# Optimization experiments

Measured on AMD Instinct MI355X. Metric: run time of the kernel, lower is better.

Reference implementation:

```python
import jax, jax.numpy as jnp
import numpy as np

B, IC, N = 32, 1, 64
KN, KS, PAD = 128, 65, 16
R, LAT = 8, 32
LEAK = 0.01
THETA_PRIOR = float(np.pi)
HW = N + 2 * PAD - KS + 1  # 32
OFFSETS = np.array([0, np.pi/4, np.pi/2, 3*np.pi/4, np.pi, -3*np.pi/4, -np.pi/2, -np.pi/4], dtype=np.float32)


def rotate_filters(w, n_rot):
    """Bilinear rotation of [O,I,k,k] filters for n_rot angles, matching
    F.affine_grid/F.grid_sample with align_corners=False, zero padding.
    Returns [O*n_rot, I, k, k] (rotation-major within each O block)."""
    O, I, k, _ = w.shape
    thetas = (2.0 * jnp.pi / n_rot) * jnp.arange(n_rot, dtype=jnp.float32)
    coords = (2.0 * jnp.arange(k, dtype=jnp.float32) + 1.0) / k - 1.0  # normalized, align_corners=False
    yy, xx = jnp.meshgrid(coords, coords, indexing='ij')  # [k,k]
    cos = jnp.cos(thetas)[:, None, None]
    sin = jnp.sin(thetas)[:, None, None]
    xs = cos * xx + sin * yy   # [R,k,k] sample x (normalized)
    ys = -sin * xx + cos * yy  # [R,k,k] sample y
    px = ((xs + 1.0) * k - 1.0) * 0.5  # pixel coords
    py = ((ys + 1.0) * k - 1.0) * 0.5
    x0 = jnp.floor(px); y0 = jnp.floor(py)
    wx = px - x0; wy = py - y0

    def gather(yi, xi):
        valid = (yi >= 0) & (yi < k) & (xi >= 0) & (xi < k)
        yc = jnp.clip(yi, 0, k - 1).astype(jnp.int32)
        xc = jnp.clip(xi, 0, k - 1).astype(jnp.int32)
        v = w[:, :, yc, xc]  # [O,I,R,k,k]
        return v * valid.astype(w.dtype)

    out = (gather(y0, x0) * (1 - wy) * (1 - wx)
           + gather(y0, x0 + 1) * (1 - wy) * wx
           + gather(y0 + 1, x0) * wy * (1 - wx)
           + gather(y0 + 1, x0 + 1) * wy * wx)  # [O,I,R,k,k]
    return jnp.transpose(out, (0, 2, 1, 3, 4)).reshape(O * n_rot, I, k, k)


def conv1x1(h, w, b):
    # h: [B,C,R,H,W], w: [O,C], b: [O] -- Conv3d with 1x1x1 kernel
    return jnp.einsum('bcrhw,oc->borhw', h, w) + b[None, :, None, None, None]


def _forward(x, w1, b1, w2, b2, wa, ba, wr, br, wz, bz, gumbel):
    tw = rotate_filters(w1[:, :, 0], R)  # [KN*R, IC, KS, KS]
    y = jax.lax.conv_general_dilated(
        x, tw, window_strides=(1, 1), padding=[(PAD, PAD), (PAD, PAD)],
        dimension_numbers=('NCHW', 'OIHW', 'NCHW'))
    Bn = y.shape[0]
    y = y.reshape(Bn, KN, R, HW, HW) + b1[None, :, None, None, None]
    xa = jax.nn.leaky_relu(y, LEAK)
    h = jax.nn.leaky_relu(conv1x1(xa, w2, b2), LEAK)
    attn = conv1x1(h, wa, ba)[:, 0]  # [B,R,H,W]
    offsets = jnp.asarray(OFFSETS)
    # Normal(0, theta_prior).log_prob(offsets)
    p_r = (-0.5 * (offsets / THETA_PRIOR) ** 2
           - jnp.log(THETA_PRIOR) - 0.5 * jnp.log(2.0 * jnp.pi))[:, None, None]  # [R,1,1]
    attn = attn + p_r  # broadcast over batch
    flat = attn.reshape(Bn, -1)
    q_t_r = jax.nn.log_softmax(flat, axis=1).reshape(attn.shape)
    a_sampled = jax.nn.softmax(flat + gumbel.reshape(Bn, -1), axis=-1).reshape(Bn, R, HW, HW)
    z = conv1x1(h, wz, bz)      # [B,2*LAT,R,H,W]
    theta = conv1x1(h, wr, br)  # [B,2,R,H,W]
    theta_mu = theta[:, 0] + offsets[None, :, None, None]
    theta = jnp.stack((theta_mu, theta[:, 1]), axis=1)
    return attn, q_t_r, p_r, a_sampled, offsets, theta, z


def setup_inputs():
    key = jax.random.key(0)
    ks = jax.random.split(key, 12)
    stdv1 = 1.0 / np.sqrt(IC * KS * KS)
    stdv2 = 1.0 / np.sqrt(KN)
    def unif(k, shape, a):
        return jax.random.uniform(k, shape, jnp.float32, -a, a)
    u = jax.random.uniform(ks[11], (B, R, HW, HW), jnp.float32, 1e-6, 1.0 - 1e-6)
    gumbel = -jnp.log(-jnp.log(u))
    return {
        'x': jax.random.normal(ks[0], (B, IC, N, N), jnp.float32),
        'w1': unif(ks[1], (KN, IC, 1, KS, KS), stdv1),
        'b1': unif(ks[2], (KN,), stdv1),
        'w2': unif(ks[3], (KN, KN), stdv2),
        'b2': unif(ks[4], (KN,), stdv2),
        'wa': unif(ks[5], (1, KN), stdv2),
        'ba': unif(ks[6], (1,), stdv2),
        'wr': unif(ks[7], (2, KN), stdv2),
        'br': unif(ks[8], (2,), stdv2),
        'wz': unif(ks[9], (2 * LAT, KN), stdv2),
        'bz': unif(ks[10], (2 * LAT,), stdv2),
        'gumbel': gumbel,
    }


def reference(x, w1, b1, w2, b2, wa, ba, wr, br, wz, bz, gumbel):
    return _forward(x, w1, b1, w2, b2, wa, ba, wr, br, wz, bz, gumbel)
```

## Files before the change

### kernel.cpp

```cpp
#include <hip/hip_runtime.h>
#include <hip/hip_bf16.h>

typedef unsigned int u32;
typedef unsigned short u16;

#define KYP 72
#define KPAD 4736
#define NK   74

#define OUT_ATTN 0
#define OUT_QTR  262144
#define OUT_PR   524288
#define OUT_AS   524296
#define OUT_OFF  786440
#define OUT_TH   786448
#define OUT_Z    1310736

typedef __attribute__((ext_vector_type(8))) short bf16x8;
typedef __attribute__((ext_vector_type(4))) float f32x4;

__device__ const float OFFS[8] = {
  0.0f,
  0.78539816339744830961f,
  1.57079632679489661923f,
  2.35619449019234492885f,
  3.14159265358979323846f,
 -2.35619449019234492885f,
 -1.57079632679489661923f,
 -0.78539816339744830961f
};

__device__ __forceinline__ float leaky_(float v){ return v >= 0.0f ? v : 0.01f*v; }

__device__ __forceinline__ u16 f2bf(float f){
  u32 x = __float_as_uint(f);
  u32 r = (x + 0x7FFFu + ((x >> 16) & 1u)) >> 16;
  return (u16)r;
}

__device__ __forceinline__ void gload_lds16(const void* g, void* l){
  __builtin_amdgcn_global_load_lds((const __attribute__((address_space(1))) u32*)g,
                                   (__attribute__((address_space(3))) u32*)l, 16, 0, 0);
}

#define BARRIER() { asm volatile("" ::: "memory"); __builtin_amdgcn_s_barrier(); asm volatile("" ::: "memory"); }
#define WAITV(N)  asm volatile("s_waitcnt vmcnt(" #N ")" ::: "memory")
#define LGK0()    { asm volatile("s_waitcnt lgkmcnt(0)" ::: "memory"); __builtin_amdgcn_sched_barrier(0); }

__global__ __launch_bounds__(256) void prep_kernel(const float* __restrict__ x, u16* __restrict__ xsh,
                                                   const float* __restrict__ w1, u16* __restrict__ twb){
  __shared__ float wsh[4225];
  if (blockIdx.x < 1024){
    int n = blockIdx.x;
    int kn = n & 127, rot = n >> 7;
    for (int i = threadIdx.x; i < 4225; i += 256) wsh[i] = w1[kn*4225 + i];
    __syncthreads();
    float th  = 0.78539816339744830961f * (float)rot;
    float cth = cosf(th), sth = sinf(th);
    for (int t = threadIdx.x; t < KPAD; t += 256){
      int ky = t / KYP, kx = t - ky*KYP;
      u16 outv = 0;
      if (ky < 65 && kx < 65){
        float yy = (2.0f*(float)ky + 1.0f)/65.0f - 1.0f;
        float xx = (2.0f*(float)kx + 1.0f)/65.0f - 1.0f;
        float xs  =  cth*xx + sth*yy;
        float ysv = -sth*xx + cth*yy;
        float px = ((xs  + 1.0f)*65.0f - 1.0f)*0.5f;
        float py = ((ysv + 1.0f)*65.0f - 1.0f)*0.5f;
        float x0 = floorf(px), y0 = floorf(py);
        float wx = px - x0, wy = py - y0;
        auto samp = [&](float yf, float xf)->float{
          bool valid = (yf >= 0.0f) && (yf < 65.0f) && (xf >= 0.0f) && (xf < 65.0f);
          int yc = (int)fminf(fmaxf(yf, 0.0f), 64.0f);
          int xc = (int)fminf(fmaxf(xf, 0.0f), 64.0f);
          return valid ? wsh[yc*65 + xc] : 0.0f;
        };
        float val = samp(y0,      x0     )*(1.0f-wy)*(1.0f-wx)
                  + samp(y0,      x0+1.0f)*(1.0f-wy)*wx
                  + samp(y0+1.0f, x0     )*wy*(1.0f-wx)
                  + samp(y0+1.0f, x0+1.0f)*wy*wx;
        outv = f2bf(val);
      }
      twb[(size_t)n*KPAD + t] = outv;
    }
  } else {
    int t = (blockIdx.x - 1024)*256 + threadIdx.x;
    if (t >= 393216) return;
    int c8  = t & 15;
    int u   = t >> 4;
    int row = u % 96;
    int v   = u / 96;
    int b   = v & 31;
    int s   = v >> 5;
    int iy = row - 16;
    u16 h[8];
#pragma unroll
    for (int j = 0; j < 8; ++j){
      int ix = c8*8 + j + s - 16;
      float val = 0.0f;
      if (iy >= 0 && iy < 64 && ix >= 0 && ix < 64) val = x[(b*64 + iy)*64 + ix];
      h[j] = f2bf(val);
    }
    uint4 pk;
    pk.x = (u32)h[0] | ((u32)h[1] << 16);
    pk.y = (u32)h[2] | ((u32)h[3] << 16);
    pk.z = (u32)h[4] | ((u32)h[5] << 16);
    pk.w = (u32)h[6] | ((u32)h[7] << 16);
    ((uint4*)xsh)[t] = pk;
  }
}

__global__ __launch_bounds__(512, 2) void gemm_kernel(const u16* __restrict__ xsh,
                                                      const u16* __restrict__ twb,
                                                      u16* __restrict__ ys){
  __shared__ u16 AsB[2*16384];
  __shared__ u16 BsB[2*16384];

  const int bid  = blockIdx.x;
  const int nblk = bid & 3, mblk = bid >> 2;
  const int t    = threadIdx.x;
  const int lane = t & 63, w = t >> 6;
  const int wr   = w >> 2, wn = w & 3;
  const int hi8  = (lane >> 4) << 3;

  const int sr  = t >> 3;
  const int j0e = (t & 7) * 8;
  const int jsw = j0e ^ ((sr & 7) << 3);
  const int bg  = mblk >> 4;
  const int ox2 = (mblk & 15) * 2;
  int aOff[4];
#pragma unroll
  for (int c = 0; c < 4; ++c){
    int i  = c*64 + sr;
    int ox = ox2 + (i >> 7);
    int s_ = ox & 7, colb = ox & ~7;
    int b_ = (bg << 2) + ((i & 127) >> 5);
    int oy = i & 31;
    aOff[c] = ((s_*32 + b_)*96 + oy)*128 + colb;
  }
  const u16* bPtr[4];
#pragma unroll
  for (int c = 0; c < 4; ++c){
    int nloc = c*64 + sr;
    bPtr[c] = twb + (size_t)(nblk*256 + nloc)*KPAD + jsw;
  }

  auto stageA4 = [&](int ky, int kx0, u16* dstbase){
    bool pad = (ky >= 65);
    int kofs = ky*128 + kx0;
#pragma unroll
    for (int c = 0; c < 4; ++c){
      int gofs = pad ? 0 : (aOff[c] + kofs);
      gload_lds16(xsh + gofs, dstbase + c*4096 + w*512);
    }
  };
  auto stageB4 = [&](int kt, u16* dstbase){
    int ktc = (kt < NK) ? kt : (NK-1);
#pragma unroll
    for (int c = 0; c < 4; ++c)
      gload_lds16(bPtr[c] + ktc*64, dstbase + c*4096 + w*512);
  };

  f32x4 acc[8][4];
#pragma unroll
  for (int i = 0; i < 8; ++i)
#pragma unroll
    for (int j = 0; j < 4; ++j) acc[i][j] = (f32x4){0.f,0.f,0.f,0.f};
  bf16x8 amat[4][2], bmat[4][2];

  auto readA = [&](int mh, const char* Ab){
#pragma unroll
    for (int mj = 0; mj < 4; ++mj){
      int row = wr*128 + mh*64 + mj*16 + (lane & 15);
#pragma unroll
      for (int kk = 0; kk < 2; ++kk){
        int off = (row*128 + (kk*32 + hi8)*2) ^ ((row & 7) << 4);
        amat[mj][kk] = *(const bf16x8*)(Ab + off);
      }
    }
  };
  auto readB = [&](int nh, const char* Bb){
#pragma unroll
    for (int jn = 0; jn < 2; ++jn){
      int row = wn*64 + (nh*2 + jn)*16 + (lane & 15);
#pragma unroll
      for (int kk = 0; kk < 2; ++kk){
        int off = (row*128 + (kk*32 + hi8)*2) ^ ((row & 7) << 4);
        bmat[nh*2 + jn][kk] = *(const bf16x8*)(Bb + off);
      }
    }
  };
  auto mfma16 = [&](int MH, int NH){
    __builtin_amdgcn_s_setprio(1);
#pragma unroll
    for (int mj = 0; mj < 4; ++mj)
#pragma unroll
      for (int jn = 0; jn < 2; ++jn)
#pragma unroll
        for (int kk = 0; kk < 2; ++kk)
          acc[MH*4+mj][NH*2+jn] = __builtin_amdgcn_mfma_f32_16x16x32_bf16(
              amat[mj][kk], bmat[NH*2+jn][kk], acc[MH*4+mj][NH*2+jn], 0, 0, 0);
    __builtin_amdgcn_s_setprio(0);
  };

  u16* const A0 = AsB;
  u16* const B0 = BsB;
  u16* const A1 = AsB + 16384;
  u16* const B1 = BsB + 16384;

  stageB4(0, B0);
  stageA4(0, jsw, A0);
  int kyN = (64 + jsw >= KYP) ? 1 : 0;
  int kxN = 64 + jsw - (kyN ? KYP : 0);
  WAITV(0);
  BARRIER();

  for (int kt = 0; kt < NK; ++kt){
    u16* Ab = (kt & 1) ? A1 : A0;
    u16* Bb = (kt & 1) ? B1 : B0;
    u16* An = (kt & 1) ? A0 : A1;
    u16* Bn = (kt & 1) ? B0 : B1;
    readA(0, (const char*)Ab); readB(0, (const char*)Bb);
    stageB4(kt+1, Bn);
    LGK0();
    mfma16(0, 0);
    readB(1, (const char*)Bb);
    stageA4(kyN, kxN, An);
    LGK0();
    mfma16(0, 1);
    readA(1, (const char*)Ab);
    LGK0();
    mfma16(1, 1);
    mfma16(1, 0);
    kxN += 64; if (kxN >= KYP){ kxN -= KYP; ++kyN; }
    WAITV(0);
    BARRIER();
  }

  const int m_base = mblk*256 + wr*128;
  const int n_base = nblk*256 + wn*64;
  const int rsub = (lane >> 4) << 2;
  const int csub = lane & 15;
#pragma unroll
  for (int mf = 0; mf < 8; ++mf)
#pragma unroll
    for (int nf = 0; nf < 4; ++nf)
#pragma unroll
      for (int j = 0; j < 4; ++j){
        int m = m_base + mf*16 + rsub + j;
        int n = n_base + nf*16 + csub;
        ys[(size_t)m*1024 + n] = f2bf(acc[mf][nf][j]);
      }
}

__global__ __launch_bounds__(512) void mix_kernel(const u16* __restrict__ ys,
    const float* __restrict__ b1, const float* __restrict__ w2, const float* __restrict__ b2,
    const float* __restrict__ wa, const float* __restrict__ ba,
    const float* __restrict__ wr, const float* __restrict__ br,
    const float* __restrict__ wz, const float* __restrict__ bz,
    float* __restrict__ out){
  __shared__ __align__(16) u16 Ah[256*128];
  __shared__ __align__(16) u16 W2s[128*128];
  __shared__ __align__(16) u16 Wcs[80*128];
  __shared__ float b2s[128];
  __shared__ float bcs[80];

  const int blk = blockIdx.x;
  const int b   = blk >> 5, oy = blk & 31;
  const int t    = threadIdx.x;
  const int lane = t & 63;
  const int w    = t >> 6;

  {
    const int kn0 = (t & 15)*8;
    const int r_  = (t >> 4) & 7;
    float b1v[8];
#pragma unroll
    for (int j = 0; j < 8; ++j) b1v[j] = b1[kn0 + j];
#pragma unroll
    for (int i = 0; i < 8; ++i){
      int m_loc = 4*i + (t >> 7);
      int row_m = (((b >> 2)*32 + m_loc)*128) + (b & 3)*32 + oy;
      uint4 v = *(const uint4*)(ys + (size_t)row_m*1024 + r_*128 + kn0);
      u32 vv[4] = {v.x, v.y, v.z, v.w};
      u16 hh[8];
#pragma unroll
      for (int j = 0; j < 4; ++j){
        float lo = __uint_as_float(vv[j] << 16);
        float hi = __uint_as_float(vv[j] & 0xFFFF0000u);
        hh[2*j]   = f2bf(leaky_(lo + b1v[2*j]));
        hh[2*j+1] = f2bf(leaky_(hi + b1v[2*j+1]));
      }
      int Arow = r_*32 + m_loc;
      int off = (Arow*256 + kn0*2) ^ ((Arow & 7) << 4);
      uint4 pk;
      pk.x = (u32)hh[0] | ((u32)hh[1] << 16);
      pk.y = (u32)hh[2] | ((u32)hh[3] << 16);
      pk.z = (u32)hh[4] | ((u32)hh[5] << 16);
      pk.w = (u32)hh[6] | ((u32)hh[7] << 16);
      *(uint4*)((char*)Ah + off) = pk;
    }
  }
#pragma unroll
  for (int i = 0; i < 4; ++i){
    int ch = i*512 + t;
    int row = ch >> 4, kn0 = (ch & 15)*8;
    const float* src = w2 + row*128 + kn0;
    u16 hh[8];
#pragma unroll
    for (int j = 0; j < 8; ++j) hh[j] = f2bf(src[j]);
    int off = (row*256 + kn0*2) ^ ((row & 7) << 4);
    uint4 pk;
    pk.x = (u32)hh[0] | ((u32)hh[1] << 16);
    pk.y = (u32)hh[2] | ((u32)hh[3] << 16);
    pk.z = (u32)hh[4] | ((u32)hh[5] << 16);
    pk.w = (u32)hh[6] | ((u32)hh[7] << 16);
    *(uint4*)((char*)W2s + off) = pk;
  }
#pragma unroll
  for (int i = 0; i < 3; ++i){
    int ch = i*512 + t;
    if (ch < 1280){
      int row = ch >> 4, kn0 = (ch & 15)*8;
      const float* src = nullptr;
      if (row < 64)      src = wz + row*128 + kn0;
      else if (row == 64) src = wa + kn0;
      else if (row == 65) src = wr + kn0;
      else if (row == 66) src = wr + 128 + kn0;
      u16 hh[8];
#pragma unroll
      for (int j = 0; j < 8; ++j) hh[j] = src ? f2bf(src[j]) : (u16)0;
      int off = (row*256 + kn0*2) ^ ((row & 7) << 4);
      uint4 pk;
      pk.x = (u32)hh[0] | ((u32)hh[1] << 16);
      pk.y = (u32)hh[2] | ((u32)hh[3] << 16);
      pk.z = (u32)hh[4] | ((u32)hh[5] << 16);
      pk.w = (u32)hh[6] | ((u32)hh[7] << 16);
      *(uint4*)((char*)Wcs + off) = pk;
    }
  }
  if (t < 128) b2s[t] = b2[t];
  if (t < 80){
    float v = 0.0f;
    if (t < 64) v = bz[t];
    else if (t == 64) v = ba[0];
    else if (t == 65) v = br[0];
    else if (t == 66) v = br[1];
    bcs[t] = v;
  }
  __syncthreads();

  f32x4 acc1[2][8];
#pragma unroll
  for (int mf = 0; mf < 2; ++mf)
#pragma unroll
    for (int nf = 0; nf < 8; ++nf) acc1[mf][nf] = (f32x4){0.f,0.f,0.f,0.f};
#pragma unroll
  for (int kk = 0; kk < 128; kk += 32){
    int kb = (kk + ((lane >> 4) << 3))*2;
    bf16x8 a[2], bv[8];
#pragma unroll
    for (int mf = 0; mf < 2; ++mf){
      int row = w*32 + mf*16 + (lane & 15);
      int off = (row*256 + kb) ^ ((row & 7) << 4);
      a[mf] = *(const bf16x8*)((const char*)Ah + off);
    }
#pragma unroll
    for (int nf = 0; nf < 8; ++nf){
      int row = nf*16 + (lane & 15);
      int off = (row*256 + kb) ^ ((row & 7) << 4);
      bv[nf] = *(const bf16x8*)((const char*)W2s + off);
    }
#pragma unroll
    for (int mf = 0; mf < 2; ++mf)
#pragma unroll
      for (int nf = 0; nf < 8; ++nf)
        acc1[mf][nf] = __builtin_amdgcn_mfma_f32_16x16x32_bf16(a[mf], bv[nf], acc1[mf][nf], 0, 0, 0);
  }
  __syncthreads();

#pragma unroll
  for (int mf = 0; mf < 2; ++mf)
#pragma unroll
    for (int nf = 0; nf < 8; ++nf){
      int col = nf*16 + (lane & 15);
      float bb = b2s[col];
#pragma unroll
      for (int j = 0; j < 4; ++j){
        int row = w*32 + mf*16 + ((lane >> 4) << 2) + j;
        u16 hv = f2bf(leaky_(acc1[mf][nf][j] + bb));
        int off = (row*256 + col*2) ^ ((row & 7) << 4);
        *(u16*)((char*)Ah + off) = hv;
      }
    }
  __syncthreads();

  f32x4 acc2[2][5];
#pragma unroll
  for (int mf = 0; mf < 2; ++mf)
#pragma unroll
    for (int nf = 0; nf < 5; ++nf) acc2[mf][nf] = (f32x4){0.f,0.f,0.f,0.f};
#pragma unroll
  for (int kk = 0; kk < 128; kk += 32){
    int kb = (kk + ((lane >> 4) << 3))*2;
    bf16x8 a[2], bv[5];
#pragma unroll
    for (int mf = 0; mf < 2; ++mf){
      int row = w*32 + mf*16 + (lane & 15);
      int off = (row*256 + kb) ^ ((row & 7) << 4);
      a[mf] = *(const bf16x8*)((const char*)Ah + off);
    }
#pragma unroll
    for (int nf = 0; nf < 5; ++nf){
      int row = nf*16 + (lane & 15);
      int off = (row*256 + kb) ^ ((row & 7) << 4);
      bv[nf] = *(const bf16x8*)((const char*)Wcs + off);
    }
#pragma unroll
    for (int mf = 0; mf < 2; ++mf)
#pragma unroll
      for (int nf = 0; nf < 5; ++nf)
        acc2[mf][nf] = __builtin_amdgcn_mfma_f32_16x16x32_bf16(a[mf], bv[nf], acc2[mf][nf], 0, 0, 0);
  }

  const int r = w;
  float off_r = OFFS[r];
  float qn = off_r / 3.14159265358979323846f;
  float pr = -0.5f*qn*qn - 1.14472988584940017414f - 0.91893853320467274178f;
  const int pixb = oy*32;
#pragma unroll
  for (int mf = 0; mf < 2; ++mf)
#pragma unroll
    for (int nf = 0; nf < 5; ++nf){
      int c = nf*16 + (lane & 15);
#pragma unroll
      for (int j = 0; j < 4; ++j){
        int ox = mf*16 + ((lane >> 4) << 2) + j;
        float val = acc2[mf][nf][j];
        if (c < 64){
          out[OUT_Z + (size_t)b*524288 + (size_t)c*8192 + r*1024 + pixb + ox] = val + bcs[c];
        } else if (c == 64){
          out[OUT_ATTN + (size_t)(b*8 + r)*1024 + pixb + ox] = val + bcs[64] + pr;
        } else if (c == 65){
          out[OUT_TH + ((size_t)b*2)*8192 + r*1024 + pixb + ox] = val + bcs[65] + off_r;
        } else if (c == 66){
          out[OUT_TH + ((size_t)b*2 + 1)*8192 + r*1024 + pixb + ox] = val + bcs[66];
        }
      }
    }
}

__global__ __launch_bounds__(1024) void softmax_kernel(const float* __restrict__ gumbel, float* __restrict__ out){
  __shared__ float a[8192];
  __shared__ float red[1024];
  const int b = blockIdx.x, t = threadIdx.x;
  if (b == 0 && t < 8){
    float off = OFFS[t];
    out[OUT_OFF + t] = off;
    float qn = off / 3.14159265358979323846f;
    out[OUT_PR + t] = -0.5f*qn*qn - 1.14472988584940017414f - 0.91893853320467274178f;
  }
  const float* attn = out + OUT_ATTN + (size_t)b*8192;
  float m = -3.0e38f;
  for (int i = t; i < 8192; i += 1024){ float v = attn[i]; a[i] = v; m = fmaxf(m, v); }
  red[t] = m; __syncthreads();
#pragma unroll
  for (int s = 512; s > 0; s >>= 1){ if (t < s) red[t] = fmaxf(red[t], red[t+s]); __syncthreads(); }
  m = red[0]; __syncthreads();
  float s1 = 0.0f;
  for (int i = t; i < 8192; i += 1024) s1 += expf(a[i] - m);
  red[t] = s1; __syncthreads();
#pragma unroll
  for (int s = 512; s > 0; s >>= 1){ if (t < s) red[t] += red[t+s]; __syncthreads(); }
  float lse = m + logf(red[0]);
  __syncthreads();
  float* q = out + OUT_QTR + (size_t)b*8192;
  for (int i = t; i < 8192; i += 1024) q[i] = a[i] - lse;
  const float* g = gumbel + (size_t)b*8192;
  float m2 = -3.0e38f;
  for (int i = t; i < 8192; i += 1024){ float v = a[i] + g[i]; a[i] = v; m2 = fmaxf(m2, v); }
  __syncthreads();
  red[t] = m2; __syncthreads();
#pragma unroll
  for (int s = 512; s > 0; s >>= 1){ if (t < s) red[t] = fmaxf(red[t], red[t+s]); __syncthreads(); }
  m2 = red[0]; __syncthreads();
  float s2 = 0.0f;
  for (int i = t; i < 8192; i += 1024) s2 += expf(a[i] - m2);
  red[t] = s2; __syncthreads();
#pragma unroll
  for (int s = 512; s > 0; s >>= 1){ if (t < s) red[t] += red[t+s]; __syncthreads(); }
  float inv = 1.0f/red[0];
  float* as_ = out + OUT_AS + (size_t)b*8192;
  for (int i = t; i < 8192; i += 1024) as_[i] = expf(a[i] - m2)*inv;
}

extern "C" void kernel_launch(void* const* d_in, const int* in_sizes, int n_in,
                              void* d_out, int out_size, void* d_ws, size_t ws_size,
                              hipStream_t stream){
  const float* x      = (const float*)d_in[0];
  const float* w1     = (const float*)d_in[1];
  const float* b1     = (const float*)d_in[2];
  const float* w2     = (const float*)d_in[3];
  const float* b2     = (const float*)d_in[4];
  const float* wa     = (const float*)d_in[5];
  const float* ba     = (const float*)d_in[6];
  const float* wr     = (const float*)d_in[7];
  const float* br     = (const float*)d_in[8];
  const float* wz     = (const float*)d_in[9];
  const float* bz     = (const float*)d_in[10];
  const float* gumbel = (const float*)d_in[11];
  float* out = (float*)d_out;

  u16* twb = (u16*)d_ws;
  u16* xsh = twb + (size_t)1024*KPAD;
  u16* ys  = xsh + (size_t)8*32*96*128;

  prep_kernel   <<<2560, 256, 0, stream>>>(x, xsh, w1, twb);
  gemm_kernel   <<<512,  512, 0, stream>>>(xsh, twb, ys);
  mix_kernel    <<<1024, 512, 0, stream>>>(ys, b1, w2, b2, wa, ba, wr, br, wz, bz, out);
  softmax_kernel<<<32,  1024, 0, stream>>>(gumbel, out);
}
```

Measured before the change: 328.2 us.

## Fuse 1x1 mixing MLP into conv GEMM epilogue, drop ys intermediate

The convolution GEMM kernel now runs the bias+leaky-ReLU, the 128x128 mixing GEMM and the 80-wide head GEMM in its epilogue. It reuses its shared-memory tiles for the activations and weights and handles its two rotations in two passes. This removes the bf16 ys round trip through global memory and the separate mix kernel launch. In exchange, every GEMM block redoes the weight staging, adds extra barriers, and raises register pressure in a kernel already bounded at 2 blocks per CU.

```diff
diff --git a/kernel.cpp b/kernel.cpp
--- a/kernel.cpp
+++ b/kernel.cpp
@@ -111,8 +111,12 @@
 }
 
 __global__ __launch_bounds__(512, 2) void gemm_kernel(const u16* __restrict__ xsh,
-                                                      const u16* __restrict__ twb,
-                                                      u16* __restrict__ ys){
+    const u16* __restrict__ twb,
+    const float* __restrict__ b1, const float* __restrict__ w2, const float* __restrict__ b2,
+    const float* __restrict__ wa, const float* __restrict__ ba,
+    const float* __restrict__ wrp, const float* __restrict__ br,
+    const float* __restrict__ wz, const float* __restrict__ bz,
+    float* __restrict__ out){
   __shared__ u16 AsB[2*16384];
   __shared__ u16 BsB[2*16384];
 
@@ -122,6 +126,8 @@
   const int lane = t & 63, w = t >> 6;
   const int wr   = w >> 2, wn = w & 3;
   const int hi8  = (lane >> 4) << 3;
+  const int rsub = (lane >> 4) << 2;
+  const int csub = lane & 15;
 
   const int sr  = t >> 3;
   const int j0e = (t & 7) * 8;
@@ -237,70 +243,12 @@
     BARRIER();
   }
 
-  const int m_base = mblk*256 + wr*128;
-  const int n_base = nblk*256 + wn*64;
-  const int rsub = (lane >> 4) << 2;
-  const int csub = lane & 15;
-#pragma unroll
-  for (int mf = 0; mf < 8; ++mf)
-#pragma unroll
-    for (int nf = 0; nf < 4; ++nf)
-#pragma unroll
-      for (int j = 0; j < 4; ++j){
-        int m = m_base + mf*16 + rsub + j;
-        int n = n_base + nf*16 + csub;
-        ys[(size_t)m*1024 + n] = f2bf(acc[mf][nf][j]);
-      }
-}
-
-__global__ __launch_bounds__(512) void mix_kernel(const u16* __restrict__ ys,
-    const float* __restrict__ b1, const float* __restrict__ w2, const float* __restrict__ b2,
-    const float* __restrict__ wa, const float* __restrict__ ba,
-    const float* __restrict__ wr, const float* __restrict__ br,
-    const float* __restrict__ wz, const float* __restrict__ bz,
-    float* __restrict__ out){
-  __shared__ __align__(16) u16 Ah[256*128];
-  __shared__ __align__(16) u16 W2s[128*128];
-  __shared__ __align__(16) u16 Wcs[80*128];
-  __shared__ float b2s[128];
-  __shared__ float bcs[80];
-
-  const int blk = blockIdx.x;
-  const int b   = blk >> 5, oy = blk & 31;
-  const int t    = threadIdx.x;
-  const int lane = t & 63;
-  const int w    = t >> 6;
-
-  {
-    const int kn0 = (t & 15)*8;
-    const int r_  = (t >> 4) & 7;
-    float b1v[8];
-#pragma unroll
-    for (int j = 0; j < 8; ++j) b1v[j] = b1[kn0 + j];
-#pragma unroll
-    for (int i = 0; i < 8; ++i){
-      int m_loc = 4*i + (t >> 7);
-      int row_m = (((b >> 2)*32 + m_loc)*128) + (b & 3)*32 + oy;
-      uint4 v = *(const uint4*)(ys + (size_t)row_m*1024 + r_*128 + kn0);
-      u32 vv[4] = {v.x, v.y, v.z, v.w};
-      u16 hh[8];
-#pragma unroll
-      for (int j = 0; j < 4; ++j){
-        float lo = __uint_as_float(vv[j] << 16);
-        float hi = __uint_as_float(vv[j] & 0xFFFF0000u);
-        hh[2*j]   = f2bf(leaky_(lo + b1v[2*j]));
-        hh[2*j+1] = f2bf(leaky_(hi + b1v[2*j+1]));
-      }
-      int Arow = r_*32 + m_loc;
-      int off = (Arow*256 + kn0*2) ^ ((Arow & 7) << 4);
-      uint4 pk;
-      pk.x = (u32)hh[0] | ((u32)hh[1] << 16);
-      pk.y = (u32)hh[2] | ((u32)hh[3] << 16);
-      pk.z = (u32)hh[4] | ((u32)hh[5] << 16);
-      pk.w = (u32)hh[6] | ((u32)hh[7] << 16);
-      *(uint4*)((char*)Ah + off) = pk;
-    }
-  }
+  u16* Ah  = AsB;
+  u16* W2s = BsB;
+  u16* Wcs = BsB + 16384;
+  float* b2s = (float*)(BsB + 26624);
+  float* bcs = b2s + 128;
+
 #pragma unroll
   for (int i = 0; i < 4; ++i){
     int ch = i*512 + t;
@@ -325,8 +273,8 @@
       const float* src = nullptr;
       if (row < 64)      src = wz + row*128 + kn0;
       else if (row == 64) src = wa + kn0;
-      else if (row == 65) src = wr + kn0;
-      else if (row == 66) src = wr + 128 + kn0;
+      else if (row == 65) src = wrp + kn0;
+      else if (row == 66) src = wrp + 128 + kn0;
       u16 hh[8];
 #pragma unroll
       for (int j = 0; j < 8; ++j) hh[j] = src ? f2bf(src[j]) : (u16)0;
@@ -348,106 +296,132 @@
     else if (t == 66) v = br[1];
     bcs[t] = v;
   }
-  __syncthreads();
-
-  f32x4 acc1[2][8];
-#pragma unroll
-  for (int mf = 0; mf < 2; ++mf)
-#pragma unroll
-    for (int nf = 0; nf < 8; ++nf) acc1[mf][nf] = (f32x4){0.f,0.f,0.f,0.f};
-#pragma unroll
-  for (int kk = 0; kk < 128; kk += 32){
-    int kb = (kk + ((lane >> 4) << 3))*2;
-    bf16x8 a[2], bv[8];
-#pragma unroll
-    for (int mf = 0; mf < 2; ++mf){
-      int row = w*32 + mf*16 + (lane & 15);
-      int off = (row*256 + kb) ^ ((row & 7) << 4);
-      a[mf] = *(const bf16x8*)((const char*)Ah + off);
-    }
-#pragma unroll
-    for (int nf = 0; nf < 8; ++nf){
-      int row = nf*16 + (lane & 15);
-      int off = (row*256 + kb) ^ ((row & 7) << 4);
-      bv[nf] = *(const bf16x8*)((const char*)W2s + off);
-    }
+
+  float b1v[4];
+#pragma unroll
+  for (int nf = 0; nf < 4; ++nf) b1v[nf] = b1[(wn & 1)*64 + nf*16 + csub];
+
+#pragma unroll 1
+  for (int p = 0; p < 2; ++p){
+    if ((wn >> 1) == p){
+#pragma unroll
+      for (int mf = 0; mf < 8; ++mf)
+#pragma unroll
+        for (int nf = 0; nf < 4; ++nf){
+          int kn = (wn & 1)*64 + nf*16 + csub;
+#pragma unroll
+          for (int j = 0; j < 4; ++j){
+            int mloc = wr*128 + mf*16 + rsub + j;
+            u16 hv = f2bf(leaky_(acc[mf][nf][j] + b1v[nf]));
+            int off = (mloc*256 + kn*2) ^ ((mloc & 7) << 4);
+            *(u16*)((char*)Ah + off) = hv;
+          }
+        }
+    }
+    __syncthreads();
+
+    f32x4 acc1[2][8];
 #pragma unroll
     for (int mf = 0; mf < 2; ++mf)
 #pragma unroll
-      for (int nf = 0; nf < 8; ++nf)
-        acc1[mf][nf] = __builtin_amdgcn_mfma_f32_16x16x32_bf16(a[mf], bv[nf], acc1[mf][nf], 0, 0, 0);
-  }
-  __syncthreads();
-
-#pragma unroll
-  for (int mf = 0; mf < 2; ++mf)
-#pragma unroll
-    for (int nf = 0; nf < 8; ++nf){
-      int col = nf*16 + (lane & 15);
-      float bb = b2s[col];
-#pragma unroll
-      for (int j = 0; j < 4; ++j){
-        int row = w*32 + mf*16 + ((lane >> 4) << 2) + j;
-        u16 hv = f2bf(leaky_(acc1[mf][nf][j] + bb));
-        int off = (row*256 + col*2) ^ ((row & 7) << 4);
-        *(u16*)((char*)Ah + off) = hv;
-      }
-    }
-  __syncthreads();
-
-  f32x4 acc2[2][5];
-#pragma unroll
-  for (int mf = 0; mf < 2; ++mf)
-#pragma unroll
-    for (int nf = 0; nf < 5; ++nf) acc2[mf][nf] = (f32x4){0.f,0.f,0.f,0.f};
-#pragma unroll
-  for (int kk = 0; kk < 128; kk += 32){
-    int kb = (kk + ((lane >> 4) << 3))*2;
-    bf16x8 a[2], bv[5];
-#pragma unroll
-    for (int mf = 0; mf < 2; ++mf){
-      int row = w*32 + mf*16 + (lane & 15);
-      int off = (row*256 + kb) ^ ((row & 7) << 4);
-      a[mf] = *(const bf16x8*)((const char*)Ah + off);
-    }
-#pragma unroll
-    for (int nf = 0; nf < 5; ++nf){
-      int row = nf*16 + (lane & 15);
-      int off = (row*256 + kb) ^ ((row & 7) << 4);
-      bv[nf] = *(const bf16x8*)((const char*)Wcs + off);
-    }
+      for (int nf = 0; nf < 8; ++nf) acc1[mf][nf] = (f32x4){0.f,0.f,0.f,0.f};
+#pragma unroll
+    for (int kk = 0; kk < 128; kk += 32){
+      int kb = (kk + hi8)*2;
+      bf16x8 a[2], bv[8];
+#pragma unroll
+      for (int mf = 0; mf < 2; ++mf){
+        int row = w*32 + mf*16 + (lane & 15);
+        int off = (row*256 + kb) ^ ((row & 7) << 4);
+        a[mf] = *(const bf16x8*)((const char*)Ah + off);
+      }
+#pragma unroll
+      for (int nf = 0; nf < 8; ++nf){
+        int row = nf*16 + (lane & 15);
+        int off = (row*256 + kb) ^ ((row & 7) << 4);
+        bv[nf] = *(const bf16x8*)((const char*)W2s + off);
+      }
+#pragma unroll
+      for (int mf = 0; mf < 2; ++mf)
+#pragma unroll
+        for (int nf = 0; nf < 8; ++nf)
+          acc1[mf][nf] = __builtin_amdgcn_mfma_f32_16x16x32_bf16(a[mf], bv[nf], acc1[mf][nf], 0, 0, 0);
+    }
+    __syncthreads();
+
 #pragma unroll
     for (int mf = 0; mf < 2; ++mf)
 #pragma unroll
-      for (int nf = 0; nf < 5; ++nf)
-        acc2[mf][nf] = __builtin_amdgcn_mfma_f32_16x16x32_bf16(a[mf], bv[nf], acc2[mf][nf], 0, 0, 0);
-  }
-
-  const int r = w;
-  float off_r = OFFS[r];
-  float qn = off_r / 3.14159265358979323846f;
-  float pr = -0.5f*qn*qn - 1.14472988584940017414f - 0.91893853320467274178f;
-  const int pixb = oy*32;
-#pragma unroll
-  for (int mf = 0; mf < 2; ++mf)
-#pragma unroll
-    for (int nf = 0; nf < 5; ++nf){
-      int c = nf*16 + (lane & 15);
-#pragma unroll
-      for (int j = 0; j < 4; ++j){
-        int ox = mf*16 + ((lane >> 4) << 2) + j;
-        float val = acc2[mf][nf][j];
-        if (c < 64){
-          out[OUT_Z + (size_t)b*524288 + (size_t)c*8192 + r*1024 + pixb + ox] = val + bcs[c];
-        } else if (c == 64){
-          out[OUT_ATTN + (size_t)(b*8 + r)*1024 + pixb + ox] = val + bcs[64] + pr;
-        } else if (c == 65){
-          out[OUT_TH + ((size_t)b*2)*8192 + r*1024 + pixb + ox] = val + bcs[65] + off_r;
-        } else if (c == 66){
-          out[OUT_TH + ((size_t)b*2 + 1)*8192 + r*1024 + pixb + ox] = val + bcs[66];
+      for (int nf = 0; nf < 8; ++nf){
+        int col = nf*16 + csub;
+        float bb = b2s[col];
+#pragma unroll
+        for (int j = 0; j < 4; ++j){
+          int row = w*32 + mf*16 + rsub + j;
+          u16 hv = f2bf(leaky_(acc1[mf][nf][j] + bb));
+          int off = (row*256 + col*2) ^ ((row & 7) << 4);
+          *(u16*)((char*)Ah + off) = hv;
         }
       }
-    }
+    __syncthreads();
+
+    f32x4 acc2[2][5];
+#pragma unroll
+    for (int mf = 0; mf < 2; ++mf)
+#pragma unroll
+      for (int nf = 0; nf < 5; ++nf) acc2[mf][nf] = (f32x4){0.f,0.f,0.f,0.f};
+#pragma unroll
+    for (int kk = 0; kk < 128; kk += 32){
+      int kb = (kk + hi8)*2;
+      bf16x8 a[2], bv[5];
+#pragma unroll
+      for (int mf = 0; mf < 2; ++mf){
+        int row = w*32 + mf*16 + (lane & 15);
+        int off = (row*256 + kb) ^ ((row & 7) << 4);
+        a[mf] = *(const bf16x8*)((const char*)Ah + off);
+      }
+#pragma unroll
+      for (int nf = 0; nf < 5; ++nf){
+        int row = nf*16 + (lane & 15);
+        int off = (row*256 + kb) ^ ((row & 7) << 4);
+        bv[nf] = *(const bf16x8*)((const char*)Wcs + off);
+      }
+#pragma unroll
+      for (int mf = 0; mf < 2; ++mf)
+#pragma unroll
+        for (int nf = 0; nf < 5; ++nf)
+          acc2[mf][nf] = __builtin_amdgcn_mfma_f32_16x16x32_bf16(a[mf], bv[nf], acc2[mf][nf], 0, 0, 0);
+    }
+    __syncthreads();
+
+    const int r = nblk*2 + p;
+    float off_r = OFFS[r];
+    float qn = off_r / 3.14159265358979323846f;
+    float pr = -0.5f*qn*qn - 1.14472988584940017414f - 0.91893853320467274178f;
+#pragma unroll
+    for (int mf = 0; mf < 2; ++mf)
+#pragma unroll
+      for (int nf = 0; nf < 5; ++nf){
+        int c = nf*16 + csub;
+#pragma unroll
+        for (int j = 0; j < 4; ++j){
+          int mloc = w*32 + mf*16 + rsub + j;
+          int oxl = mloc >> 7, b_ = (mloc & 127) >> 5, oy = mloc & 31;
+          int pix = oy*32 + ox2 + oxl;
+          int bf_ = bg*4 + b_;
+          float val = acc2[mf][nf][j];
+          if (c < 64){
+            out[OUT_Z + (size_t)bf_*524288 + (size_t)c*8192 + r*1024 + pix] = val + bcs[c];
+          } else if (c == 64){
+            out[OUT_ATTN + (size_t)(bf_*8 + r)*1024 + pix] = val + bcs[64] + pr;
+          } else if (c == 65){
+            out[OUT_TH + ((size_t)bf_*2)*8192 + r*1024 + pix] = val + bcs[65] + off_r;
+          } else if (c == 66){
+            out[OUT_TH + ((size_t)bf_*2 + 1)*8192 + r*1024 + pix] = val + bcs[66];
+          }
+        }
+      }
+  }
 }
 
 __global__ __launch_bounds__(1024) void softmax_kernel(const float* __restrict__ gumbel, float* __restrict__ out){
@@ -513,10 +487,8 @@
 
   u16* twb = (u16*)d_ws;
   u16* xsh = twb + (size_t)1024*KPAD;
-  u16* ys  = xsh + (size_t)8*32*96*128;
 
   prep_kernel   <<<2560, 256, 0, stream>>>(x, xsh, w1, twb);
-  gemm_kernel   <<<512,  512, 0, stream>>>(xsh, twb, ys);
-  mix_kernel    <<<1024, 512, 0, stream>>>(ys, b1, w2, b2, wa, ba, wr, br, wz, bz, out);
+  gemm_kernel   <<<512,  512, 0, stream>>>(xsh, twb, b1, w2, b2, wa, ba, wr, br, wz, bz, out);
   softmax_kernel<<<32,  1024, 0, stream>>>(gumbel, out);
 }
```

Result: slower. 613.8 us (+87.0%).
